# Optimization experiments

Measured on AMD Instinct MI355X. Metric: run time of the kernel, lower is better.

## Reference

```python
import jax, jax.numpy as jnp
import numpy as np

STATE_DIM = 512
MAX_STEPS = 16
BATCH = 4096
NOISE_SCALE = 0.1


def setup_inputs() -> dict:
    key = jax.random.key(0)
    ks = jax.random.split(key, 12)
    D = STATE_DIM
    init = lambda k, shape, scale: (jax.random.normal(k, shape, dtype=jnp.float32) * scale)
    inp = {
        'initial_state': init(ks[0], (BATCH, D), 1.0),
        'noise': init(ks[1], (MAX_STEPS, BATCH, D), 1.0),
        # initial_v_proj: Linear(D, D)
        'Wv': init(ks[2], (D, D), 0.02), 'bv': jnp.zeros((D,), jnp.float32),
        # evidence_transform: Linear(2D, D) -> tanh -> Linear(D, D)
        'W1': init(ks[3], (D, 2 * D), 0.02), 'b1': jnp.zeros((D,), jnp.float32),
        'W2': init(ks[4], (D, D), 0.02), 'b2': jnp.zeros((D,), jnp.float32),
        # noise_gate: Linear(1,32) -> ReLU -> Linear(32,1) -> Sigmoid
        'Wg1': init(ks[5], (32, 1), 0.5), 'bg1': jnp.zeros((32,), jnp.float32),
        'Wg2': init(ks[6], (1, 32), 0.5), 'bg2': jnp.zeros((1,), jnp.float32),
        # clamped scalar params
        'raw_decay': jnp.float32(0.9),
        'raw_dt': jnp.float32(0.1),
        'raw_spring': jnp.float32(0.5),
        'raw_threshold': jnp.float32(0.05),
    }
    return inp


def reference(initial_state, noise, Wv, bv, W1, b1, W2, b2, Wg1, bg1, Wg2, bg2,
              raw_decay, raw_dt, raw_spring, raw_threshold):
    decay = jnp.clip(raw_decay, 0.5, 0.99)
    dt = jnp.clip(raw_dt, 0.01, 0.5)
    spring = jnp.abs(raw_spring) + 0.01
    threshold = jnp.abs(raw_threshold) + 0.0001

    x0 = initial_state
    v0 = initial_state @ Wv.T + bv  # initial_v_proj

    def step(carry, noise_t):
        x, v = carry
        gz = jnp.linalg.norm(v, axis=-1, keepdims=True)  # (B,1)
        # hopfield is None -> retrieved = zeros_like(x)
        evidence_in = jnp.concatenate([x, jnp.zeros_like(x)], axis=-1)  # (B,2D)
        force = spring * (jnp.tanh(evidence_in @ W1.T + b1) @ W2.T + b2)
        gate = jax.nn.sigmoid(jax.nn.relu(gz @ Wg1.T + bg1) @ Wg2.T + bg2)  # (B,1)
        v_new = decay * v + force + noise_t * gate * NOISE_SCALE
        x_new = x + dt * v_new
        return (x_new, v_new), (x_new, v_new, jnp.mean(gz[:, 0]))

    (xf, vf), (xs, vs, gzs) = jax.lax.scan(step, (x0, v0), noise)
    positions = jnp.concatenate([x0[None], xs], axis=0)    # (17, B, D)
    velocities = jnp.concatenate([v0[None], vs], axis=0)   # (17, B, D)
    gray_zones = jnp.concatenate(
        [jnp.mean(jnp.linalg.norm(v0, axis=-1))[None], gzs], axis=0)  # (17,)
    converged = jnp.linalg.norm(vf, axis=-1) < jax.lax.stop_gradient(threshold)
    return xf, vf, positions, velocities, gray_zones, converged
```

## Files before the change

kernel.cpp:

```cpp
#include <hip/hip_runtime.h>
#include <hip/hip_bf16.h>

#define DIM      512
#define NSTEPS   16
#define BATCH    4096

#define OFF_XF   0
#define OFF_VF   2097152
#define OFF_POS  4194304
#define OFF_VEL  39845888
#define OFF_GZ   75497472
#define OFF_CONV 75497489
#define SLAB     2097152

#define WS_WV 0
#define WS_W1 524288
#define WS_W2 1048576
#define WS_GZ 1572864

#define TOT_TILES 528

typedef __attribute__((ext_vector_type(8))) short short8v;
typedef __attribute__((ext_vector_type(4))) float f32x4;

__device__ __forceinline__ unsigned short f2bf(float f) {
  union { float f; unsigned u; } a; a.f = f;
  return (unsigned short)((a.u + 0x7FFFu + ((a.u >> 16) & 1u)) >> 16);
}

__device__ __forceinline__ float tanh_fast(float x) {
  float e = __expf(2.0f * x);
  return 1.0f - 2.0f / (e + 1.0f);
}

__device__ __forceinline__ void st_bf(unsigned short* lds, int r, int c, float f) {
  int byte = (c << 1) ^ ((r & 7) << 4);
  *(unsigned short*)((char*)lds + (r << 10) + byte) = f2bf(f);
}

__global__ void prep_kernel(const float* __restrict__ Wv,
                            const float* __restrict__ W1,
                            const float* __restrict__ W2,
                            unsigned short* __restrict__ ws) {
  int t = blockIdx.x * 256 + threadIdx.x;
  if (t < 32) ((float*)(ws + WS_GZ / 2))[t] = 0.0f;
  int mat = t >> 15, idx = t & 32767;
  int lane = idx & 63, nt = (idx >> 6) & 31, T = idx >> 11;
  const float* W = (mat == 0) ? Wv : (mat == 1) ? W1 : W2;
  int stride = (mat == 1) ? 1024 : 512;
  unsigned short* o = ws + (mat == 0 ? WS_WV / 2 : (mat == 1) ? WS_W1 / 2 : WS_W2 / 2);
  int row = nt * 16 + (lane & 15);
  int col = T * 32 + (lane >> 4) * 8;
  const float* src = W + row * stride + col;
  short8v v;
#pragma unroll
  for (int j = 0; j < 8; ++j) v[j] = (short)f2bf(src[j]);
  *(short8v*)(o + ((T * 32 + nt) * 64 + lane) * 8) = v;
}

__device__ __forceinline__ void issue_tile(int abs2, const char* wsv, const char* ws1,
                                           const char* ws2, unsigned short* lds_b,
                                           int w2048, int lane16) {
  if (abs2 >= TOT_TILES) return;
  const char* mb; int T;
  if (abs2 < 16) { mb = wsv; T = abs2; }
  else { int rel = abs2 - 16; T = rel & 15; mb = ((rel >> 4) & 1) ? ws2 : ws1; }
  const char* src = mb + (T << 15) + w2048 + lane16;
  char* dst = (char*)lds_b + (abs2 % 3) * 32768 + w2048;
  __builtin_amdgcn_global_load_lds(
      (const __attribute__((address_space(1))) void*)src,
      (__attribute__((address_space(3))) void*)dst, 16, 0, 0);
  __builtin_amdgcn_global_load_lds(
      (const __attribute__((address_space(1))) void*)(src + 1024),
      (__attribute__((address_space(3))) void*)(dst + 1024), 16, 0, 0);
}

__device__ __forceinline__ void tile_compute(int bufi, int T, const unsigned short* lds_b,
                                             const char* aptr, int acol0, int aswz,
                                             int boff, f32x4* acc) {
  short8v a = *(const short8v*)(aptr + ((T * 64 + acol0) ^ aswz));
  const unsigned short* bb = lds_b + bufi * 16384 + boff;
  short8v b0 = *(const short8v*)(bb);
  short8v b1 = *(const short8v*)(bb + 512);
  acc[0] = __builtin_amdgcn_mfma_f32_16x16x32_bf16(a, b0, acc[0], 0, 0, 0);
  acc[1] = __builtin_amdgcn_mfma_f32_16x16x32_bf16(a, b1, acc[1], 0, 0, 0);
}

#define WAITV(n) asm volatile("s_waitcnt vmcnt(" #n ")" ::: "memory")
#define LGKM0    asm volatile("s_waitcnt lgkmcnt(0)" ::: "memory")
#define BAR      __builtin_amdgcn_s_barrier()

__launch_bounds__(1024, 4)
__global__ void main_kernel(const float* __restrict__ x0,
                            const float* __restrict__ noise,
                            const float* __restrict__ bv,
                            const float* __restrict__ b1,
                            const float* __restrict__ b2,
                            const float* __restrict__ Wg1,
                            const float* __restrict__ bg1,
                            const float* __restrict__ Wg2,
                            const float* __restrict__ bg2,
                            const float* __restrict__ rdecay,
                            const float* __restrict__ rdt,
                            const float* __restrict__ rspring,
                            const float* __restrict__ rthr,
                            const unsigned short* __restrict__ ws,
                            float* __restrict__ gzsum,
                            float* __restrict__ out) {
  __shared__ unsigned short lds_b[49152];
  __shared__ unsigned short a_lds[8192];
  __shared__ float gz_p[16];
  __shared__ float gate_lds[16];

  const int tid  = threadIdx.x;
  const int lane = tid & 63;
  const int w    = tid >> 6;
  const int lg   = lane >> 4;
  const int li   = lane & 15;
  const int base = blockIdx.x * 16;

  const char* wsv = (const char*)ws + WS_WV;
  const char* ws1 = (const char*)ws + WS_W1;
  const char* ws2 = (const char*)ws + WS_W2;
  const int w2048  = w * 2048;
  const int lane16 = lane * 16;
  const char* aptr = (const char*)a_lds + li * 1024;
  const int acol0 = lg * 16;
  const int aswz  = (li & 7) << 4;
  const int boff  = w * 1024 + lane * 8;

  issue_tile(0, wsv, ws1, ws2, lds_b, w2048, lane16);
  issue_tile(1, wsv, ws1, ws2, lds_b, w2048, lane16);

  const float decay  = fminf(fmaxf(rdecay[0], 0.5f), 0.99f);
  const float dt     = fminf(fmaxf(rdt[0], 0.01f), 0.5f);
  const float spring = fabsf(rspring[0]) + 0.01f;

  int colv[2], rowv[4], rg[4];
  float b1c[2], b2c[2], bvc[2];
#pragma unroll
  for (int q = 0; q < 2; ++q) {
    colv[q] = w * 32 + q * 16 + li;
    b1c[q] = b1[colv[q]]; b2c[q] = b2[colv[q]]; bvc[q] = bv[colv[q]];
  }
#pragma unroll
  for (int j = 0; j < 4; ++j) { rowv[j] = lg * 4 + j; rg[j] = (base + rowv[j]) * DIM; }

  if (tid < 16) gz_p[tid] = 0.0f;
  for (int i = tid; i < 2048; i += 1024) {
    int r = i >> 7, c4 = (i & 127) * 4;
    f32x4 xv = *(const f32x4*)&x0[(base + r) * DIM + c4];
    st_bf(a_lds, r, c4 + 0, xv.x); st_bf(a_lds, r, c4 + 1, xv.y);
    st_bf(a_lds, r, c4 + 2, xv.z); st_bf(a_lds, r, c4 + 3, xv.w);
    *(f32x4*)&out[OFF_POS + (size_t)(base + r) * DIM + c4] = xv;
  }
  float x[2][4], v[2][4];
#pragma unroll
  for (int q = 0; q < 2; ++q)
#pragma unroll
    for (int j = 0; j < 4; ++j) x[q][j] = x0[rg[j] + colv[q]];
  LGKM0; BAR;

  f32x4 acc[2];
  acc[0] = (f32x4){0.f, 0.f, 0.f, 0.f};
  acc[1] = (f32x4){0.f, 0.f, 0.f, 0.f};
#pragma unroll
  for (int T = 0; T < 16; ++T) {
    issue_tile(T + 2, wsv, ws1, ws2, lds_b, w2048, lane16);
    WAITV(4);
    tile_compute(T % 3, T, lds_b, aptr, acol0, aswz, boff, acc);
  }
#pragma unroll
  for (int q = 0; q < 2; ++q)
#pragma unroll
    for (int j = 0; j < 4; ++j) {
      v[q][j] = acc[q][j] + bvc[q];
      out[OFF_VEL + rg[j] + colv[q]] = v[q][j];
    }

  for (int t = 0; t < NSTEPS; ++t) {
    const int sb = 16 + t * 32;

    BAR;
    if (t > 0) {
#pragma unroll
      for (int q = 0; q < 2; ++q)
#pragma unroll
        for (int j = 0; j < 4; ++j) st_bf(a_lds, rowv[j], colv[q], x[q][j]);
    }
    float nz[2][4];
    {
      const float* np = noise + (size_t)t * (BATCH * DIM);
#pragma unroll
      for (int q = 0; q < 2; ++q)
#pragma unroll
        for (int j = 0; j < 4; ++j) nz[q][j] = np[rg[j] + colv[q]];
    }
#pragma unroll
    for (int j = 0; j < 4; ++j) {
      float s = 0.f;
#pragma unroll
      for (int q = 0; q < 2; ++q) s += v[q][j] * v[q][j];
      s += __shfl_xor(s, 1); s += __shfl_xor(s, 2);
      s += __shfl_xor(s, 4); s += __shfl_xor(s, 8);
      if (li == 0) atomicAdd(&gz_p[rowv[j]], s);
    }
    LGKM0; BAR;

    if (tid < 16) {
      float g = sqrtf(gz_p[tid]);
      gz_p[tid] = 0.0f;
      float z = bg2[0];
#pragma unroll
      for (int k = 0; k < 32; ++k) {
        float a = fmaxf(fmaf(g, Wg1[k], bg1[k]), 0.0f);
        z = fmaf(Wg2[k], a, z);
      }
      gate_lds[tid] = 1.0f / (1.0f + __expf(-z));
      float bs = g;
      bs += __shfl_xor(bs, 1); bs += __shfl_xor(bs, 2);
      bs += __shfl_xor(bs, 4); bs += __shfl_xor(bs, 8);
      if (tid == 0) {
        atomicAdd(&gzsum[t + 1], bs);
        if (t == 0) atomicAdd(&gzsum[0], bs);
      }
    }
    LGKM0; BAR;

    acc[0] = (f32x4){0.f, 0.f, 0.f, 0.f};
    acc[1] = (f32x4){0.f, 0.f, 0.f, 0.f};
#pragma unroll
    for (int T = 0; T < 16; ++T) {
      issue_tile(sb + T + 2, wsv, ws1, ws2, lds_b, w2048, lane16);
      WAITV(4);
      tile_compute((sb + T) % 3, T, lds_b, aptr, acol0, aswz, boff, acc);
    }
    BAR;
#pragma unroll
    for (int q = 0; q < 2; ++q)
#pragma unroll
      for (int j = 0; j < 4; ++j)
        st_bf(a_lds, rowv[j], colv[q], tanh_fast(acc[q][j] + b1c[q]));
    LGKM0; BAR;

    acc[0] = (f32x4){0.f, 0.f, 0.f, 0.f};
    acc[1] = (f32x4){0.f, 0.f, 0.f, 0.f};
#pragma unroll
    for (int T = 0; T < 16; ++T) {
      issue_tile(sb + 18 + T, wsv, ws1, ws2, lds_b, w2048, lane16);
      if (t == NSTEPS - 1 && T >= 14) {
        if (T == 14) { WAITV(2); } else { WAITV(0); }
      } else {
        WAITV(4);
      }
      tile_compute((sb + 16 + T) % 3, T, lds_b, aptr, acol0, aswz, boff, acc);
    }

    float* pos = out + OFF_POS + (size_t)(t + 1) * SLAB;
    float* vel = out + OFF_VEL + (size_t)(t + 1) * SLAB;
#pragma unroll
    for (int j = 0; j < 4; ++j) {
      float g = gate_lds[rowv[j]];
#pragma unroll
      for (int q = 0; q < 2; ++q) {
        float force = spring * (acc[q][j] + b2c[q]);
        float vn = fmaf(decay, v[q][j], force) + nz[q][j] * g * 0.1f;
        v[q][j] = vn;
        x[q][j] = fmaf(dt, vn, x[q][j]);
        int gi = rg[j] + colv[q];
        pos[gi] = x[q][j];
        vel[gi] = vn;
        if (t == NSTEPS - 1) { out[OFF_XF + gi] = x[q][j]; out[OFF_VF + gi] = vn; }
      }
    }
  }

#pragma unroll
  for (int j = 0; j < 4; ++j) {
    float s = 0.f;
#pragma unroll
    for (int q = 0; q < 2; ++q) s += v[q][j] * v[q][j];
    s += __shfl_xor(s, 1); s += __shfl_xor(s, 2);
    s += __shfl_xor(s, 4); s += __shfl_xor(s, 8);
    if (li == 0) atomicAdd(&gz_p[rowv[j]], s);
  }
  LGKM0; BAR;
  if (tid < 16) {
    float thr = fabsf(rthr[0]) + 1e-4f;
    out[OFF_CONV + base + tid] = (sqrtf(gz_p[tid]) < thr) ? 1.0f : 0.0f;
  }
}

__global__ void finalize_kernel(const float* __restrict__ gzsum,
                                float* __restrict__ out) {
  int t = threadIdx.x;
  if (t < 17) out[OFF_GZ + t] = gzsum[t] * (1.0f / 4096.0f);
}

extern "C" void kernel_launch(void* const* d_in, const int* in_sizes, int n_in,
                              void* d_out, int out_size, void* d_ws, size_t ws_size,
                              hipStream_t stream) {
  const float* x0     = (const float*)d_in[0];
  const float* noise  = (const float*)d_in[1];
  const float* Wv     = (const float*)d_in[2];
  const float* bv     = (const float*)d_in[3];
  const float* W1     = (const float*)d_in[4];
  const float* b1     = (const float*)d_in[5];
  const float* W2     = (const float*)d_in[6];
  const float* b2     = (const float*)d_in[7];
  const float* Wg1    = (const float*)d_in[8];
  const float* bg1    = (const float*)d_in[9];
  const float* Wg2    = (const float*)d_in[10];
  const float* bg2    = (const float*)d_in[11];
  const float* rdec   = (const float*)d_in[12];
  const float* rdt    = (const float*)d_in[13];
  const float* rspr   = (const float*)d_in[14];
  const float* rthr   = (const float*)d_in[15];
  unsigned short* ws  = (unsigned short*)d_ws;
  float* gz           = (float*)((char*)d_ws + WS_GZ);
  float* out          = (float*)d_out;

  prep_kernel<<<384, 256, 0, stream>>>(Wv, W1, W2, ws);
  main_kernel<<<256, 1024, 0, stream>>>(x0, noise, bv, b1, b2, Wg1, bg1, Wg2, bg2,
                                        rdec, rdt, rspr, rthr, ws, gz, out);
  finalize_kernel<<<1, 32, 0, stream>>>(gz, out);
}
```

Measured before the change: 660.6 us.

## Process 32 rows per block to double weight-tile reuse per MFMA

Each block now handles 32 batch rows with a 2x2 accumulator layout, so each streamed weight tile from LDS feeds four MFMAs instead of two. The grid halves to 128 blocks and total weight traffic from L2 halves. The trade-off is that only half the compute units are occupied, and per-block work and register use grow.

```diff
diff --git a/kernel.cpp b/kernel.cpp
--- a/kernel.cpp
+++ b/kernel.cpp
@@ -43,7 +43,7 @@
                             const float* __restrict__ W2,
                             unsigned short* __restrict__ ws) {
   int t = blockIdx.x * 256 + threadIdx.x;
-  if (t < 32) ((float*)(ws + WS_GZ / 2))[t] = 0.0f;
+  if (t < 64) ((float*)(ws + WS_GZ / 2))[t] = 0.0f;
   int mat = t >> 15, idx = t & 32767;
   int lane = idx & 63, nt = (idx >> 6) & 31, T = idx >> 11;
   const float* W = (mat == 0) ? Wv : (mat == 1) ? W1 : W2;
@@ -76,55 +76,63 @@
 }
 
 __device__ __forceinline__ void tile_compute(int bufi, int T, const unsigned short* lds_b,
-                                             const char* aptr, int acol0, int aswz,
-                                             int boff, f32x4* acc) {
-  short8v a = *(const short8v*)(aptr + ((T * 64 + acol0) ^ aswz));
+                                             const char* aptr0, const char* aptr1,
+                                             int acol0, int aswz, int boff, f32x4 acc[2][2]) {
+  int aoff = (T * 64 + acol0) ^ aswz;
+  short8v a0 = *(const short8v*)(aptr0 + aoff);
+  short8v a1 = *(const short8v*)(aptr1 + aoff);
   const unsigned short* bb = lds_b + bufi * 16384 + boff;
   short8v b0 = *(const short8v*)(bb);
   short8v b1 = *(const short8v*)(bb + 512);
-  acc[0] = __builtin_amdgcn_mfma_f32_16x16x32_bf16(a, b0, acc[0], 0, 0, 0);
-  acc[1] = __builtin_amdgcn_mfma_f32_16x16x32_bf16(a, b1, acc[1], 0, 0, 0);
+  acc[0][0] = __builtin_amdgcn_mfma_f32_16x16x32_bf16(a0, b0, acc[0][0], 0, 0, 0);
+  acc[0][1] = __builtin_amdgcn_mfma_f32_16x16x32_bf16(a0, b1, acc[0][1], 0, 0, 0);
+  acc[1][0] = __builtin_amdgcn_mfma_f32_16x16x32_bf16(a1, b0, acc[1][0], 0, 0, 0);
+  acc[1][1] = __builtin_amdgcn_mfma_f32_16x16x32_bf16(a1, b1, acc[1][1], 0, 0, 0);
 }
 
 #define WAITV(n) asm volatile("s_waitcnt vmcnt(" #n ")" ::: "memory")
 #define LGKM0    asm volatile("s_waitcnt lgkmcnt(0)" ::: "memory")
 #define BAR      __builtin_amdgcn_s_barrier()
 
-__launch_bounds__(1024, 4)
-__global__ void main_kernel(const float* __restrict__ x0,
-                            const float* __restrict__ noise,
-                            const float* __restrict__ bv,
-                            const float* __restrict__ b1,
-                            const float* __restrict__ b2,
-                            const float* __restrict__ Wg1,
-                            const float* __restrict__ bg1,
-                            const float* __restrict__ Wg2,
-                            const float* __restrict__ bg2,
-                            const float* __restrict__ rdecay,
-                            const float* __restrict__ rdt,
-                            const float* __restrict__ rspring,
-                            const float* __restrict__ rthr,
-                            const unsigned short* __restrict__ ws,
-                            float* __restrict__ gzsum,
-                            float* __restrict__ out) {
+#define ZACC do { acc[0][0] = (f32x4){0.f,0.f,0.f,0.f}; acc[0][1] = (f32x4){0.f,0.f,0.f,0.f}; \
+                  acc[1][0] = (f32x4){0.f,0.f,0.f,0.f}; acc[1][1] = (f32x4){0.f,0.f,0.f,0.f}; } while (0)
+
+__global__ __launch_bounds__(1024)
+void main_kernel(const float* __restrict__ x0,
+                 const float* __restrict__ noise,
+                 const float* __restrict__ bv,
+                 const float* __restrict__ b1,
+                 const float* __restrict__ b2,
+                 const float* __restrict__ Wg1,
+                 const float* __restrict__ bg1,
+                 const float* __restrict__ Wg2,
+                 const float* __restrict__ bg2,
+                 const float* __restrict__ rdecay,
+                 const float* __restrict__ rdt,
+                 const float* __restrict__ rspring,
+                 const float* __restrict__ rthr,
+                 const unsigned short* __restrict__ ws,
+                 float* __restrict__ gzsum,
+                 float* __restrict__ out) {
   __shared__ unsigned short lds_b[49152];
-  __shared__ unsigned short a_lds[8192];
-  __shared__ float gz_p[16];
-  __shared__ float gate_lds[16];
+  __shared__ unsigned short a_lds[16384];
+  __shared__ float gz_p[32];
+  __shared__ float gate_lds[32];
 
   const int tid  = threadIdx.x;
   const int lane = tid & 63;
   const int w    = tid >> 6;
   const int lg   = lane >> 4;
   const int li   = lane & 15;
-  const int base = blockIdx.x * 16;
+  const int base = blockIdx.x * 32;
 
   const char* wsv = (const char*)ws + WS_WV;
   const char* ws1 = (const char*)ws + WS_W1;
   const char* ws2 = (const char*)ws + WS_W2;
   const int w2048  = w * 2048;
   const int lane16 = lane * 16;
-  const char* aptr = (const char*)a_lds + li * 1024;
+  const char* aptr0 = (const char*)a_lds + li * 1024;
+  const char* aptr1 = (const char*)a_lds + (16 + li) * 1024;
   const int acol0 = lg * 16;
   const int aswz  = (li & 7) << 4;
   const int boff  = w * 1024 + lane * 8;
@@ -136,47 +144,56 @@
   const float dt     = fminf(fmaxf(rdt[0], 0.01f), 0.5f);
   const float spring = fabsf(rspring[0]) + 0.01f;
 
-  int colv[2], rowv[4], rg[4];
+  int colv[2];
   float b1c[2], b2c[2], bvc[2];
 #pragma unroll
   for (int q = 0; q < 2; ++q) {
     colv[q] = w * 32 + q * 16 + li;
     b1c[q] = b1[colv[q]]; b2c[q] = b2[colv[q]]; bvc[q] = bv[colv[q]];
   }
-#pragma unroll
-  for (int j = 0; j < 4; ++j) { rowv[j] = lg * 4 + j; rg[j] = (base + rowv[j]) * DIM; }
-
-  if (tid < 16) gz_p[tid] = 0.0f;
-  for (int i = tid; i < 2048; i += 1024) {
+  int rowv[2][4], rg[2][4];
+#pragma unroll
+  for (int m = 0; m < 2; ++m)
+#pragma unroll
+    for (int j = 0; j < 4; ++j) {
+      rowv[m][j] = m * 16 + lg * 4 + j;
+      rg[m][j] = (base + rowv[m][j]) * DIM;
+    }
+
+  if (tid < 32) gz_p[tid] = 0.0f;
+  for (int i = tid; i < 4096; i += 1024) {
     int r = i >> 7, c4 = (i & 127) * 4;
     f32x4 xv = *(const f32x4*)&x0[(base + r) * DIM + c4];
     st_bf(a_lds, r, c4 + 0, xv.x); st_bf(a_lds, r, c4 + 1, xv.y);
     st_bf(a_lds, r, c4 + 2, xv.z); st_bf(a_lds, r, c4 + 3, xv.w);
     *(f32x4*)&out[OFF_POS + (size_t)(base + r) * DIM + c4] = xv;
   }
-  float x[2][4], v[2][4];
-#pragma unroll
-  for (int q = 0; q < 2; ++q)
-#pragma unroll
-    for (int j = 0; j < 4; ++j) x[q][j] = x0[rg[j] + colv[q]];
+  float x[2][2][4], v[2][2][4];
+#pragma unroll
+  for (int m = 0; m < 2; ++m)
+#pragma unroll
+    for (int q = 0; q < 2; ++q)
+#pragma unroll
+      for (int j = 0; j < 4; ++j) x[m][q][j] = x0[rg[m][j] + colv[q]];
   LGKM0; BAR;
 
-  f32x4 acc[2];
-  acc[0] = (f32x4){0.f, 0.f, 0.f, 0.f};
-  acc[1] = (f32x4){0.f, 0.f, 0.f, 0.f};
+  f32x4 acc[2][2];
+  ZACC;
 #pragma unroll
   for (int T = 0; T < 16; ++T) {
     issue_tile(T + 2, wsv, ws1, ws2, lds_b, w2048, lane16);
     WAITV(4);
-    tile_compute(T % 3, T, lds_b, aptr, acol0, aswz, boff, acc);
-  }
-#pragma unroll
-  for (int q = 0; q < 2; ++q)
-#pragma unroll
-    for (int j = 0; j < 4; ++j) {
-      v[q][j] = acc[q][j] + bvc[q];
-      out[OFF_VEL + rg[j] + colv[q]] = v[q][j];
-    }
+    tile_compute(T % 3, T, lds_b, aptr0, aptr1, acol0, aswz, boff, acc);
+  }
+#pragma unroll
+  for (int m = 0; m < 2; ++m)
+#pragma unroll
+    for (int q = 0; q < 2; ++q)
+#pragma unroll
+      for (int j = 0; j < 4; ++j) {
+        v[m][q][j] = acc[m][q][j] + bvc[q];
+        out[OFF_VEL + rg[m][j] + colv[q]] = v[m][q][j];
+      }
 
   for (int t = 0; t < NSTEPS; ++t) {
     const int sb = 16 + t * 32;
@@ -184,30 +201,36 @@
     BAR;
     if (t > 0) {
 #pragma unroll
-      for (int q = 0; q < 2; ++q)
-#pragma unroll
-        for (int j = 0; j < 4; ++j) st_bf(a_lds, rowv[j], colv[q], x[q][j]);
-    }
-    float nz[2][4];
+      for (int m = 0; m < 2; ++m)
+#pragma unroll
+        for (int q = 0; q < 2; ++q)
+#pragma unroll
+          for (int j = 0; j < 4; ++j) st_bf(a_lds, rowv[m][j], colv[q], x[m][q][j]);
+    }
+    float nz[2][2][4];
     {
       const float* np = noise + (size_t)t * (BATCH * DIM);
 #pragma unroll
-      for (int q = 0; q < 2; ++q)
-#pragma unroll
-        for (int j = 0; j < 4; ++j) nz[q][j] = np[rg[j] + colv[q]];
-    }
-#pragma unroll
-    for (int j = 0; j < 4; ++j) {
-      float s = 0.f;
-#pragma unroll
-      for (int q = 0; q < 2; ++q) s += v[q][j] * v[q][j];
-      s += __shfl_xor(s, 1); s += __shfl_xor(s, 2);
-      s += __shfl_xor(s, 4); s += __shfl_xor(s, 8);
-      if (li == 0) atomicAdd(&gz_p[rowv[j]], s);
-    }
+      for (int m = 0; m < 2; ++m)
+#pragma unroll
+        for (int q = 0; q < 2; ++q)
+#pragma unroll
+          for (int j = 0; j < 4; ++j) nz[m][q][j] = np[rg[m][j] + colv[q]];
+    }
+#pragma unroll
+    for (int m = 0; m < 2; ++m)
+#pragma unroll
+      for (int j = 0; j < 4; ++j) {
+        float s = 0.f;
+#pragma unroll
+        for (int q = 0; q < 2; ++q) s += v[m][q][j] * v[m][q][j];
+        s += __shfl_xor(s, 1); s += __shfl_xor(s, 2);
+        s += __shfl_xor(s, 4); s += __shfl_xor(s, 8);
+        if (li == 0) atomicAdd(&gz_p[rowv[m][j]], s);
+      }
     LGKM0; BAR;
 
-    if (tid < 16) {
+    if (tid < 32) {
       float g = sqrtf(gz_p[tid]);
       gz_p[tid] = 0.0f;
       float z = bg2[0];
@@ -220,6 +243,7 @@
       float bs = g;
       bs += __shfl_xor(bs, 1); bs += __shfl_xor(bs, 2);
       bs += __shfl_xor(bs, 4); bs += __shfl_xor(bs, 8);
+      bs += __shfl_xor(bs, 16);
       if (tid == 0) {
         atomicAdd(&gzsum[t + 1], bs);
         if (t == 0) atomicAdd(&gzsum[0], bs);
@@ -227,24 +251,24 @@
     }
     LGKM0; BAR;
 
-    acc[0] = (f32x4){0.f, 0.f, 0.f, 0.f};
-    acc[1] = (f32x4){0.f, 0.f, 0.f, 0.f};
+    ZACC;
 #pragma unroll
     for (int T = 0; T < 16; ++T) {
       issue_tile(sb + T + 2, wsv, ws1, ws2, lds_b, w2048, lane16);
       WAITV(4);
-      tile_compute((sb + T) % 3, T, lds_b, aptr, acol0, aswz, boff, acc);
+      tile_compute((sb + T) % 3, T, lds_b, aptr0, aptr1, acol0, aswz, boff, acc);
     }
     BAR;
 #pragma unroll
-    for (int q = 0; q < 2; ++q)
-#pragma unroll
-      for (int j = 0; j < 4; ++j)
-        st_bf(a_lds, rowv[j], colv[q], tanh_fast(acc[q][j] + b1c[q]));
+    for (int m = 0; m < 2; ++m)
+#pragma unroll
+      for (int q = 0; q < 2; ++q)
+#pragma unroll
+        for (int j = 0; j < 4; ++j)
+          st_bf(a_lds, rowv[m][j], colv[q], tanh_fast(acc[m][q][j] + b1c[q]));
     LGKM0; BAR;
 
-    acc[0] = (f32x4){0.f, 0.f, 0.f, 0.f};
-    acc[1] = (f32x4){0.f, 0.f, 0.f, 0.f};
+    ZACC;
 #pragma unroll
     for (int T = 0; T < 16; ++T) {
       issue_tile(sb + 18 + T, wsv, ws1, ws2, lds_b, w2048, lane16);
@@ -253,39 +277,43 @@
       } else {
         WAITV(4);
       }
-      tile_compute((sb + 16 + T) % 3, T, lds_b, aptr, acol0, aswz, boff, acc);
+      tile_compute((sb + 16 + T) % 3, T, lds_b, aptr0, aptr1, acol0, aswz, boff, acc);
     }
 
     float* pos = out + OFF_POS + (size_t)(t + 1) * SLAB;
     float* vel = out + OFF_VEL + (size_t)(t + 1) * SLAB;
 #pragma unroll
+    for (int m = 0; m < 2; ++m)
+#pragma unroll
+      for (int j = 0; j < 4; ++j) {
+        float g = gate_lds[rowv[m][j]];
+#pragma unroll
+        for (int q = 0; q < 2; ++q) {
+          float force = spring * (acc[m][q][j] + b2c[q]);
+          float vn = fmaf(decay, v[m][q][j], force) + nz[m][q][j] * g * 0.1f;
+          v[m][q][j] = vn;
+          x[m][q][j] = fmaf(dt, vn, x[m][q][j]);
+          int gi = rg[m][j] + colv[q];
+          pos[gi] = x[m][q][j];
+          vel[gi] = vn;
+          if (t == NSTEPS - 1) { out[OFF_XF + gi] = x[m][q][j]; out[OFF_VF + gi] = vn; }
+        }
+      }
+  }
+
+#pragma unroll
+  for (int m = 0; m < 2; ++m)
+#pragma unroll
     for (int j = 0; j < 4; ++j) {
-      float g = gate_lds[rowv[j]];
-#pragma unroll
-      for (int q = 0; q < 2; ++q) {
-        float force = spring * (acc[q][j] + b2c[q]);
-        float vn = fmaf(decay, v[q][j], force) + nz[q][j] * g * 0.1f;
-        v[q][j] = vn;
-        x[q][j] = fmaf(dt, vn, x[q][j]);
-        int gi = rg[j] + colv[q];
-        pos[gi] = x[q][j];
-        vel[gi] = vn;
-        if (t == NSTEPS - 1) { out[OFF_XF + gi] = x[q][j]; out[OFF_VF + gi] = vn; }
-      }
-    }
-  }
-
-#pragma unroll
-  for (int j = 0; j < 4; ++j) {
-    float s = 0.f;
-#pragma unroll
-    for (int q = 0; q < 2; ++q) s += v[q][j] * v[q][j];
-    s += __shfl_xor(s, 1); s += __shfl_xor(s, 2);
-    s += __shfl_xor(s, 4); s += __shfl_xor(s, 8);
-    if (li == 0) atomicAdd(&gz_p[rowv[j]], s);
-  }
+      float s = 0.f;
+#pragma unroll
+      for (int q = 0; q < 2; ++q) s += v[m][q][j] * v[m][q][j];
+      s += __shfl_xor(s, 1); s += __shfl_xor(s, 2);
+      s += __shfl_xor(s, 4); s += __shfl_xor(s, 8);
+      if (li == 0) atomicAdd(&gz_p[rowv[m][j]], s);
+    }
   LGKM0; BAR;
-  if (tid < 16) {
+  if (tid < 32) {
     float thr = fabsf(rthr[0]) + 1e-4f;
     out[OFF_CONV + base + tid] = (sqrtf(gz_p[tid]) < thr) ? 1.0f : 0.0f;
   }
@@ -321,7 +349,7 @@
   float* out          = (float*)d_out;
 
   prep_kernel<<<384, 256, 0, stream>>>(Wv, W1, W2, ws);
-  main_kernel<<<256, 1024, 0, stream>>>(x0, noise, bv, b1, b2, Wg1, bg1, Wg2, bg2,
+  main_kernel<<<128, 1024, 0, stream>>>(x0, noise, bv, b1, b2, Wg1, bg1, Wg2, bg2,
                                         rdec, rdt, rspr, rthr, ws, gz, out);
   finalize_kernel<<<1, 32, 0, stream>>>(gz, out);
 }
```

Result: slower. 979.6 us (+48.3%).
